# Kernel optimization log

Hardware: AMD Instinct MI355X
Metric: run time of the kernel (lower is better)

## Reference

```python
import jax, jax.numpy as jnp
import numpy as np

ROUTE_SCALE = 2.5
TOP_K = 2
N_EXPERTS = 16


def setup_inputs() -> dict:
    key = jax.random.key(0)
    ks = jax.random.split(key, 8)
    B, T, D, I, E = 2, 1024, 768, 384, N_EXPERTS
    s = 0.02
    return {
        "x": jax.random.normal(ks[0], (B, T, D), dtype=jnp.float32),
        "gate_w": jax.random.normal(ks[1], (E, D), dtype=jnp.float32) * s,
        "sg_w": jax.random.normal(ks[2], (I, D), dtype=jnp.float32) * s,
        "su_w": jax.random.normal(ks[3], (I, D), dtype=jnp.float32) * s,
        "sd_w": jax.random.normal(ks[4], (D, I), dtype=jnp.float32) * s,
        "rg_w": jax.random.normal(ks[5], (E, I, D), dtype=jnp.float32) * s,
        "ru_w": jax.random.normal(ks[6], (E, I, D), dtype=jnp.float32) * s,
        "rd_w": jax.random.normal(ks[7], (E, D, I), dtype=jnp.float32) * s,
    }


def _moe_forward(x, gate_w, sg_w, su_w, sd_w, rg_w, ru_w, rd_w):
    B, T, D = x.shape
    flat = x.reshape(-1, D)  # (N, D), N = B*T

    # ---- shared expert (SwiGLU FFN) ----
    g = flat @ sg_w.T
    u = flat @ su_w.T
    shared_out = (jax.nn.silu(g) * u) @ sd_w.T  # (N, D)

    # ---- gate: softmax(fp32) -> top-k -> renormalize ----
    logits = (flat @ gate_w.T) * ROUTE_SCALE  # (N, E)
    scores = jax.nn.softmax(logits.astype(jnp.float32), axis=-1)
    topk_w, topk_i = jax.lax.top_k(scores, TOP_K)  # (N, K)
    topk_w = topk_w / jnp.sum(topk_w, axis=-1, keepdims=True)
    topk_w = topk_w.astype(x.dtype)

    # aux load-balancing loss
    one_hot = jax.nn.one_hot(topk_i, N_EXPERTS, dtype=jnp.float32)  # (N, K, E)
    mask = one_hot.sum(axis=1)  # (N, E)
    f = mask.mean(axis=0)
    p = scores.mean(axis=0)
    aux_loss = jnp.sum(f * p) * N_EXPERTS

    # combine weights per (token, expert): sum_k w_k * [idx_k == e]
    combine = jnp.einsum("nk,nke->ne", topk_w, one_hot.astype(x.dtype))  # (N, E)

    # ---- routed experts as batched (grouped) SwiGLU GEMMs ----
    rg = jnp.einsum("nd,eid->nei", flat, rg_w)  # (N, E, I)
    ru = jnp.einsum("nd,eid->nei", flat, ru_w)
    rh = jax.nn.silu(rg) * ru  # (N, E, I)
    eo = jnp.einsum("nei,edi->ned", rh, rd_w)  # (N, E, D)
    routed_out = jnp.einsum("ned,ne->nd", eo, combine)  # (N, D)

    out = (shared_out + routed_out).reshape(B, T, D)
    return out, aux_loss


def reference(x, gate_w, sg_w, su_w, sd_w, rg_w, ru_w, rd_w):
    return _moe_forward(x, gate_w, sg_w, su_w, sd_w, rg_w, ru_w, rd_w)
```

## Files before the change

### kernel.cpp

```cpp
#include <hip/hip_runtime.h>
#include <math.h>

#define NTOK 2048
#define DDIM 768
#define IDIM 384
#define NEXP 16
#define ECAP 2048
#define HSHARED (NEXP * ECAP)
#define GBLK (NTOK / 4)

#define MT 64
#define NSHT2 32
#define NRT2 80
#define NW2 ((NSHT2 + NRT2) * 6)
#define CH2 (NW2 / 8)

#define CR_Z0 1
#define CR_X0 (CR_Z0 + 384)
#define CR_W10 (CR_X0 + 192)
#define CR_WD0 (CR_W10 + 816)
#define CR_END (CR_WD0 + 816)

typedef __attribute__((ext_vector_type(8))) short short8;
typedef __attribute__((ext_vector_type(4))) float f32x4;

__device__ __forceinline__ unsigned short f2bf(float f) {
    unsigned int u = __float_as_uint(f);
    unsigned int r = (u + 0x7fffu + ((u >> 16) & 1u)) >> 16;
    return (unsigned short)r;
}

__device__ __forceinline__ void gload16(const void* g, void* l) {
    __builtin_amdgcn_global_load_lds(
        (const __attribute__((address_space(1))) void*)g,
        (__attribute__((address_space(3))) void*)l, 16, 0, 0);
}

#define WS_XB   1048576u
#define WS_W1F  4194304u
#define WS_WDF  24248320u
#define WS_H    34275328u

__global__ __launch_bounds__(256) void gate_kernel(
    const float* __restrict__ x, const float* __restrict__ gate_w,
    int* __restrict__ topk_i, float* __restrict__ topk_w,
    float* __restrict__ p_partial) {
    __shared__ float p_blk[16];
    int tid = threadIdx.x;
    if (tid < 16) p_blk[tid] = 0.f;
    __syncthreads();

    int wave = tid >> 6, lane = tid & 63;
    int n = blockIdx.x * 4 + wave;
    int e = lane >> 2, q = lane & 3;
    const float4* xr = (const float4*)(x + (size_t)n * DDIM);
    const float4* wr = (const float4*)(gate_w + (size_t)e * DDIM);
    float s = 0.f;
    #pragma unroll 4
    for (int k = q * 48; k < q * 48 + 48; ++k) {
        float4 a = xr[k], b = wr[k];
        s += a.x * b.x + a.y * b.y + a.z * b.z + a.w * b.w;
    }
    s += __shfl_xor(s, 1);
    s += __shfl_xor(s, 2);
    float logit = s * 2.5f;

    float m = logit;
    #pragma unroll
    for (int mask = 4; mask < 64; mask <<= 1)
        m = fmaxf(m, __shfl_xor(m, mask));
    float ex = __expf(logit - m);
    float sum = ex;
    #pragma unroll
    for (int mask = 4; mask < 64; mask <<= 1)
        sum += __shfl_xor(sum, mask);
    float sc = ex / sum;

    float v = sc; int idx = e;
    #pragma unroll
    for (int mask = 4; mask < 64; mask <<= 1) {
        float ov = __shfl_xor(v, mask);
        int   oi = __shfl_xor(idx, mask);
        if (ov > v || (ov == v && oi < idx)) { v = ov; idx = oi; }
    }
    float b0 = v; int i0 = idx;
    v = (e == i0) ? -1.f : sc; idx = e;
    #pragma unroll
    for (int mask = 4; mask < 64; mask <<= 1) {
        float ov = __shfl_xor(v, mask);
        int   oi = __shfl_xor(idx, mask);
        if (ov > v || (ov == v && oi < idx)) { v = ov; idx = oi; }
    }
    float b1 = v; int i1 = idx;
    float rs = 1.f / (b0 + b1);

    if (lane == 0) {
        topk_i[n * 2] = i0; topk_i[n * 2 + 1] = i1;
        topk_w[n * 2] = b0 * rs; topk_w[n * 2 + 1] = b1 * rs;
    }
    if (q == 0) atomicAdd(&p_blk[e], sc);
    __syncthreads();
    if (tid < 16) p_partial[blockIdx.x * 16 + tid] = p_blk[tid];
}

__global__ __launch_bounds__(256) void convroute_kernel(
    const float* __restrict__ x,
    const float* __restrict__ rgw, const float* __restrict__ ruw,
    const float* __restrict__ sgw, const float* __restrict__ suw,
    const float* __restrict__ rdw, const float* __restrict__ sdw,
    float4* __restrict__ out4,
    unsigned short* __restrict__ xb, unsigned short* __restrict__ w1f,
    unsigned short* __restrict__ wdf,
    const int* __restrict__ topk_i, const float* __restrict__ topk_w,
    const float* __restrict__ p_partial,
    int* __restrict__ counts, int* __restrict__ perm_t, float* __restrict__ perm_w,
    float* __restrict__ out_aux) {
    __shared__ unsigned short sbuf[16 * 780];
    int b = blockIdx.x, tid = threadIdx.x;

    if (b == 0) {
        float* s_p    = (float*)sbuf;
        float* s_psum = s_p + 256;
        int*   s_cnt  = (int*)(s_psum + 16);
        int*   s_cur  = s_cnt + 16;
        {
            int e = tid & 15, g = tid >> 4;
            float acc = 0.f;
            for (int bb = g; bb < GBLK; bb += 16) acc += p_partial[bb * 16 + e];
            s_p[tid] = acc;
        }
        if (tid < 16) { s_cnt[tid] = 0; s_cur[tid] = 0; }
        __syncthreads();
        if (tid < 16) {
            float a = 0.f;
            #pragma unroll
            for (int g = 0; g < 16; ++g) a += s_p[g * 16 + tid];
            s_psum[tid] = a;
        }
        for (int n = tid; n < NTOK; n += 256) {
            atomicAdd(&s_cnt[topk_i[n * 2]], 1);
            atomicAdd(&s_cnt[topk_i[n * 2 + 1]], 1);
        }
        __syncthreads();
        if (tid < 16) counts[tid] = s_cnt[tid];
        if (tid == 0) {
            float a = 0.f;
            for (int e = 0; e < 16; ++e) a += (float)s_cnt[e] * s_psum[e];
            out_aux[0] = a * 16.f / ((float)NTOK * (float)NTOK);
        }
        for (int n = tid; n < NTOK; n += 256) {
            #pragma unroll
            for (int k = 0; k < 2; ++k) {
                int e = topk_i[n * 2 + k];
                int pos = atomicAdd(&s_cur[e], 1);
                perm_t[e * ECAP + pos] = n;
                perm_w[e * ECAP + pos] = topk_w[n * 2 + k];
            }
        }
        return;
    }

    if (b < CR_X0) {
        float4 z = make_float4(0.f, 0.f, 0.f, 0.f);
        float4* dst = out4 + (b - CR_Z0) * 1024 + tid;
        #pragma unroll
        for (int j = 0; j < 4; ++j) dst[j * 256] = z;
        return;
    }

    if (b < CR_W10) {
        int bb = b - CR_X0;
        #pragma unroll
        for (int j = 0; j < 4; ++j) {
            int i = bb * 1024 + j * 256 + tid;
            const float* s = x + (size_t)i * 8;
            float4 v0 = *(const float4*)s, v1 = *(const float4*)(s + 4);
            short8 o;
            o[0]=f2bf(v0.x); o[1]=f2bf(v0.y); o[2]=f2bf(v0.z); o[3]=f2bf(v0.w);
            o[4]=f2bf(v1.x); o[5]=f2bf(v1.y); o[6]=f2bf(v1.z); o[7]=f2bf(v1.w);
            *(short8*)(xb + (size_t)i * 8) = o;
        }
        return;
    }

    if (b < CR_WD0) {
        int bb = b - CR_W10;
        int E = bb / 48, rg = bb % 48;
        const float* gsrc_ = (E == 16) ? sgw : rgw + (size_t)E * (IDIM * DDIM);
        const float* usrc_ = (E == 16) ? suw : ruw + (size_t)E * (IDIM * DDIM);
        const float* src = ((rg & 1) ? usrc_ : gsrc_) + (size_t)(rg >> 1) * 16 * DDIM;
        #pragma unroll
        for (int i = 0; i < 12; ++i) {
            int idx = i * 256 + tid;
            int r = idx / 192, c4 = idx - r * 192;
            float4 v = ((const float4*)(src + (size_t)r * DDIM))[c4];
            ushort4 o4;
            o4.x = f2bf(v.x); o4.y = f2bf(v.y); o4.z = f2bf(v.z); o4.w = f2bf(v.w);
            *(ushort4*)(sbuf + r * 780 + c4 * 4) = o4;
        }
        __syncthreads();
        unsigned short* wbase = w1f + (size_t)E * (DDIM * DDIM) + (size_t)rg * 24 * 512;
        #pragma unroll
        for (int c = 0; c < 6; ++c) {
            int cc = c * 256 + tid;
            int ks = cc >> 6, l = cc & 63;
            short8 v8 = *(const short8*)(sbuf + (l & 15) * 780 + ks * 32 + (l >> 4) * 8);
            *(short8*)(wbase + (size_t)(ks * 64 + l) * 8) = v8;
        }
        return;
    }

    {
        int bb = b - CR_WD0;
        int E = bb / 48, cg = bb % 48;
        const float* src = ((E == 16) ? sdw : rdw + (size_t)E * (DDIM * IDIM))
                         + (size_t)cg * 16 * IDIM;
        #pragma unroll
        for (int i = 0; i < 6; ++i) {
            int idx = i * 256 + tid;
            int r = idx / 96, c4 = idx - r * 96;
            float4 v = ((const float4*)(src + (size_t)r * IDIM))[c4];
            ushort4 o4;
            o4.x = f2bf(v.x); o4.y = f2bf(v.y); o4.z = f2bf(v.z); o4.w = f2bf(v.w);
            *(ushort4*)(sbuf + r * 390 + c4 * 4) = o4;
        }
        __syncthreads();
        unsigned short* wbase = wdf + (size_t)E * (DDIM * IDIM) + (size_t)cg * 12 * 512;
        #pragma unroll
        for (int c = 0; c < 3; ++c) {
            int cc = c * 256 + tid;
            int ks = cc >> 6, l = cc & 63;
            short8 v8 = *(const short8*)(sbuf + (l & 15) * 390 + ks * 32 + (l >> 4) * 8);
            *(short8*)(wbase + (size_t)(ks * 64 + l) * 8) = v8;
        }
    }
}

__device__ __forceinline__ void swz_decode(int lid, int& bx, int& y) {
    int wid = (lid & 7) * CH2 + (lid >> 3);
    bx = wid / 6;
    y = wid - bx * 6;
}

__device__ __forceinline__ bool tile_decode(const int* __restrict__ counts,
                                            int r, int& e, int& t, int& cnt) {
    int acc = 0;
    for (int ee = 0; ee < NEXP; ++ee) {
        int c = counts[ee];
        int tiles = (c + 63) >> 6;
        if (r < acc + tiles) { e = ee; t = r - acc; cnt = c; return true; }
        acc += tiles;
    }
    return false;
}

__global__ __launch_bounds__(256, 4) void p1_kernel(
    const unsigned short* __restrict__ xb, const unsigned short* __restrict__ w1f,
    const int* __restrict__ counts, const int* __restrict__ perm_t,
    unsigned short* __restrict__ h) {
    __shared__ unsigned short xs[24 * 512];
    __shared__ int s_tok[MT];

    int tid = threadIdx.x;
    int bx, y;
    swz_decode(blockIdx.x, bx, y);
    int e, hbase;
    if (bx < NSHT2) {
        e = 16;
        hbase = HSHARED + bx * MT;
        if (tid < MT) s_tok[tid] = bx * MT + tid;
    } else {
        int t, cnt;
        if (!tile_decode(counts, bx - NSHT2, e, t, cnt)) return;
        hbase = e * ECAP + t * MT;
        if (tid < MT) {
            int slot = t * MT + tid;
            s_tok[tid] = (slot < cnt) ? perm_t[e * ECAP + slot] : 0;
        }
    }
    __syncthreads();

    int lane = tid & 63, wave = tid >> 6;
    int lr = lane & 15, kg8 = (lane >> 4) * 8, jrow = (lane >> 4) * 4;

    const unsigned short* gsrc = xb + (size_t)s_tok[wave * 16 + lr] * DDIM + kg8;

    const unsigned short* pg = w1f + ((((size_t)e * 48 + (y * 8 + wave * 2    )) * 24) * 64 + lane) * 8;
    const unsigned short* pu = w1f + ((((size_t)e * 48 + (y * 8 + wave * 2 + 1)) * 24) * 64 + lane) * 8;

    f32x4 ag0 = (f32x4)0.f, ag1 = (f32x4)0.f, ag2 = (f32x4)0.f, ag3 = (f32x4)0.f;
    f32x4 au0 = (f32x4)0.f, au1 = (f32x4)0.f, au2 = (f32x4)0.f, au3 = (f32x4)0.f;

    for (int ch = 0; ch < 4; ++ch) {
        if (ch) __syncthreads();
        #pragma unroll
        for (int c = 0; c < 6; ++c)
            gload16(gsrc + (ch * 6 + c) * 32, &xs[(wave * 6 + c) * 512]);
        __syncthreads();

        #pragma unroll
        for (int ksl = 0; ksl < 6; ++ksl) {
            int ksg = ch * 6 + ksl;
            short8 bg = *(const short8*)(pg + (size_t)ksg * 512);
            short8 bu = *(const short8*)(pu + (size_t)ksg * 512);
            short8 a0 = *(const short8*)(xs + (     ksl) * 512 + lane * 8);
            short8 a1 = *(const short8*)(xs + ( 6 + ksl) * 512 + lane * 8);
            short8 a2 = *(const short8*)(xs + (12 + ksl) * 512 + lane * 8);
            short8 a3 = *(const short8*)(xs + (18 + ksl) * 512 + lane * 8);
            ag0 = __builtin_amdgcn_mfma_f32_16x16x32_bf16(a0, bg, ag0, 0, 0, 0);
            au0 = __builtin_amdgcn_mfma_f32_16x16x32_bf16(a0, bu, au0, 0, 0, 0);
            ag1 = __builtin_amdgcn_mfma_f32_16x16x32_bf16(a1, bg, ag1, 0, 0, 0);
            au1 = __builtin_amdgcn_mfma_f32_16x16x32_bf16(a1, bu, au1, 0, 0, 0);
            ag2 = __builtin_amdgcn_mfma_f32_16x16x32_bf16(a2, bg, ag2, 0, 0, 0);
            au2 = __builtin_amdgcn_mfma_f32_16x16x32_bf16(a2, bu, au2, 0, 0, 0);
            ag3 = __builtin_amdgcn_mfma_f32_16x16x32_bf16(a3, bg, ag3, 0, 0, 0);
            au3 = __builtin_amdgcn_mfma_f32_16x16x32_bf16(a3, bu, au3, 0, 0, 0);
        }
    }

    int colg = y * 64 + wave * 16 + lr;
    #pragma unroll
    for (int mf = 0; mf < 4; ++mf) {
        f32x4 g4 = (mf == 0) ? ag0 : (mf == 1) ? ag1 : (mf == 2) ? ag2 : ag3;
        f32x4 u4 = (mf == 0) ? au0 : (mf == 1) ? au1 : (mf == 2) ? au2 : au3;
        #pragma unroll
        for (int j = 0; j < 4; ++j) {
            int tl = mf * 16 + jrow + j;
            float g = g4[j], u = u4[j];
            float hv = g / (1.f + __expf(-g)) * u;
            h[(size_t)(hbase + tl) * IDIM + colg] = f2bf(hv);
        }
    }
}

__global__ __launch_bounds__(256, 4) void p2_kernel(
    const unsigned short* __restrict__ h, const unsigned short* __restrict__ wdf,
    const int* __restrict__ counts,
    const int* __restrict__ perm_t, const float* __restrict__ perm_w,
    float* __restrict__ out) {
    __shared__ unsigned short hs[24 * 512];
    __shared__ int   s_tok[MT];
    __shared__ float s_w[MT];

    int tid = threadIdx.x;
    int bx, y;
    swz_decode(blockIdx.x, bx, y);
    int e, hbase;
    if (bx < NSHT2) {
        e = 16;
        hbase = HSHARED + bx * MT;
        if (tid < MT) { s_tok[tid] = bx * MT + tid; s_w[tid] = 1.f; }
    } else {
        int t, cnt;
        if (!tile_decode(counts, bx - NSHT2, e, t, cnt)) return;
        hbase = e * ECAP + t * MT;
        if (tid < MT) {
            int slot = t * MT + tid;
            bool v = slot < cnt;
            s_tok[tid] = v ? perm_t[e * ECAP + slot] : 0;
            s_w[tid]   = v ? perm_w[e * ECAP + slot] : 0.f;
        }
    }
    __syncthreads();

    int lane = tid & 63, wave = tid >> 6;
    int lr = lane & 15, kg8 = (lane >> 4) * 8, jrow = (lane >> 4) * 4;

    const unsigned short* gsrc = h + (size_t)(hbase + wave * 16 + lr) * IDIM + kg8;

    const unsigned short* p0 = wdf + ((((size_t)e * 48 + (y * 8 + wave * 2    )) * 12) * 64 + lane) * 8;
    const unsigned short* p1 = wdf + ((((size_t)e * 48 + (y * 8 + wave * 2 + 1)) * 12) * 64 + lane) * 8;

    f32x4 c00 = (f32x4)0.f, c01 = (f32x4)0.f, c02 = (f32x4)0.f, c03 = (f32x4)0.f;
    f32x4 c10 = (f32x4)0.f, c11 = (f32x4)0.f, c12 = (f32x4)0.f, c13 = (f32x4)0.f;

    for (int ch = 0; ch < 2; ++ch) {
        if (ch) __syncthreads();
        #pragma unroll
        for (int c = 0; c < 6; ++c)
            gload16(gsrc + (ch * 6 + c) * 32, &hs[(wave * 6 + c) * 512]);
        __syncthreads();

        #pragma unroll
        for (int ksl = 0; ksl < 6; ++ksl) {
            int ksg = ch * 6 + ksl;
            short8 b0 = *(const short8*)(p0 + (size_t)ksg * 512);
            short8 b1 = *(const short8*)(p1 + (size_t)ksg * 512);
            short8 a0 = *(const short8*)(hs + (     ksl) * 512 + lane * 8);
            short8 a1 = *(const short8*)(hs + ( 6 + ksl) * 512 + lane * 8);
            short8 a2 = *(const short8*)(hs + (12 + ksl) * 512 + lane * 8);
            short8 a3 = *(const short8*)(hs + (18 + ksl) * 512 + lane * 8);
            c00 = __builtin_amdgcn_mfma_f32_16x16x32_bf16(a0, b0, c00, 0, 0, 0);
            c10 = __builtin_amdgcn_mfma_f32_16x16x32_bf16(a0, b1, c10, 0, 0, 0);
            c01 = __builtin_amdgcn_mfma_f32_16x16x32_bf16(a1, b0, c01, 0, 0, 0);
            c11 = __builtin_amdgcn_mfma_f32_16x16x32_bf16(a1, b1, c11, 0, 0, 0);
            c02 = __builtin_amdgcn_mfma_f32_16x16x32_bf16(a2, b0, c02, 0, 0, 0);
            c12 = __builtin_amdgcn_mfma_f32_16x16x32_bf16(a2, b1, c12, 0, 0, 0);
            c03 = __builtin_amdgcn_mfma_f32_16x16x32_bf16(a3, b0, c03, 0, 0, 0);
            c13 = __builtin_amdgcn_mfma_f32_16x16x32_bf16(a3, b1, c13, 0, 0, 0);
        }
    }

    int col0 = y * 128 + wave * 32 + lr;
    #pragma unroll
    for (int mf = 0; mf < 4; ++mf) {
        f32x4 v0 = (mf == 0) ? c00 : (mf == 1) ? c01 : (mf == 2) ? c02 : c03;
        f32x4 v1 = (mf == 0) ? c10 : (mf == 1) ? c11 : (mf == 2) ? c12 : c13;
        #pragma unroll
        for (int j = 0; j < 4; ++j) {
            int tl = mf * 16 + jrow + j;
            float w = s_w[tl];
            if (w == 0.f) continue;
            float* orow = out + (size_t)s_tok[tl] * DDIM;
            atomicAdd(orow + col0,      w * v0[j]);
            atomicAdd(orow + col0 + 16, w * v1[j]);
        }
    }
}

extern "C" void kernel_launch(void* const* d_in, const int* in_sizes, int n_in,
                              void* d_out, int out_size, void* d_ws, size_t ws_size,
                              hipStream_t stream) {
    const float* x      = (const float*)d_in[0];
    const float* gate_w = (const float*)d_in[1];
    const float* sg_w   = (const float*)d_in[2];
    const float* su_w   = (const float*)d_in[3];
    const float* sd_w   = (const float*)d_in[4];
    const float* rg_w   = (const float*)d_in[5];
    const float* ru_w   = (const float*)d_in[6];
    const float* rd_w   = (const float*)d_in[7];
    float* out = (float*)d_out;

    char* ws = (char*)d_ws;
    int*   counts    = (int*)(ws + 0);
    int*   perm_t    = (int*)(ws + 1024);
    float* perm_w    = (float*)(ws + 132096);
    float* p_partial = (float*)(ws + 263168);
    int*   topk_i    = (int*)(ws + 295936);
    float* topk_w    = (float*)(ws + 312320);
    unsigned short* xb  = (unsigned short*)(ws + WS_XB);
    unsigned short* w1f = (unsigned short*)(ws + WS_W1F);
    unsigned short* wdf = (unsigned short*)(ws + WS_WDF);
    unsigned short* hbuf= (unsigned short*)(ws + WS_H);

    gate_kernel<<<GBLK, 256, 0, stream>>>(x, gate_w, topk_i, topk_w, p_partial);

    convroute_kernel<<<CR_END, 256, 0, stream>>>(
        x, rg_w, ru_w, sg_w, su_w, rd_w, sd_w,
        (float4*)out, xb, w1f, wdf,
        topk_i, topk_w, p_partial, counts, perm_t, perm_w,
        out + (size_t)NTOK * DDIM);

    p1_kernel<<<NW2, 256, 0, stream>>>(xb, w1f, counts, perm_t, hbuf);

    p2_kernel<<<NW2, 256, 0, stream>>>(hbuf, wdf, counts, perm_t, perm_w, out);
}
```

Baseline: 97.37 us.

## Load GEMM A-operands directly from global memory instead of staging through LDS

Both expert GEMM kernels stop copying the token/activation tile into shared memory with global_load_lds and barriers. Each wave now reads its A fragments straight from global memory, with the K loop fully unrolled. This removes the LDS staging, the __syncthreads and the LDS footprint, which may raise occupancy. In exchange every wave redundantly fetches the same 64-row A tile from global/L2, which raises cache traffic fourfold for the A operand.

```diff
diff --git a/kernel.cpp b/kernel.cpp
--- a/kernel.cpp
+++ b/kernel.cpp
@@ -28,12 +28,6 @@
     unsigned int u = __float_as_uint(f);
     unsigned int r = (u + 0x7fffu + ((u >> 16) & 1u)) >> 16;
     return (unsigned short)r;
-}
-
-__device__ __forceinline__ void gload16(const void* g, void* l) {
-    __builtin_amdgcn_global_load_lds(
-        (const __attribute__((address_space(1))) void*)g,
-        (__attribute__((address_space(3))) void*)l, 16, 0, 0);
 }
 
 #define WS_XB   1048576u
@@ -258,7 +252,6 @@
     const unsigned short* __restrict__ xb, const unsigned short* __restrict__ w1f,
     const int* __restrict__ counts, const int* __restrict__ perm_t,
     unsigned short* __restrict__ h) {
-    __shared__ unsigned short xs[24 * 512];
     __shared__ int s_tok[MT];
 
     int tid = threadIdx.x;
@@ -283,7 +276,10 @@
     int lane = tid & 63, wave = tid >> 6;
     int lr = lane & 15, kg8 = (lane >> 4) * 8, jrow = (lane >> 4) * 4;
 
-    const unsigned short* gsrc = xb + (size_t)s_tok[wave * 16 + lr] * DDIM + kg8;
+    const unsigned short* pa0 = xb + (size_t)s_tok[     lr] * DDIM + kg8;
+    const unsigned short* pa1 = xb + (size_t)s_tok[16 + lr] * DDIM + kg8;
+    const unsigned short* pa2 = xb + (size_t)s_tok[32 + lr] * DDIM + kg8;
+    const unsigned short* pa3 = xb + (size_t)s_tok[48 + lr] * DDIM + kg8;
 
     const unsigned short* pg = w1f + ((((size_t)e * 48 + (y * 8 + wave * 2    )) * 24) * 64 + lane) * 8;
     const unsigned short* pu = w1f + ((((size_t)e * 48 + (y * 8 + wave * 2 + 1)) * 24) * 64 + lane) * 8;
@@ -291,31 +287,22 @@
     f32x4 ag0 = (f32x4)0.f, ag1 = (f32x4)0.f, ag2 = (f32x4)0.f, ag3 = (f32x4)0.f;
     f32x4 au0 = (f32x4)0.f, au1 = (f32x4)0.f, au2 = (f32x4)0.f, au3 = (f32x4)0.f;
 
-    for (int ch = 0; ch < 4; ++ch) {
-        if (ch) __syncthreads();
-        #pragma unroll
-        for (int c = 0; c < 6; ++c)
-            gload16(gsrc + (ch * 6 + c) * 32, &xs[(wave * 6 + c) * 512]);
-        __syncthreads();
-
-        #pragma unroll
-        for (int ksl = 0; ksl < 6; ++ksl) {
-            int ksg = ch * 6 + ksl;
-            short8 bg = *(const short8*)(pg + (size_t)ksg * 512);
-            short8 bu = *(const short8*)(pu + (size_t)ksg * 512);
-            short8 a0 = *(const short8*)(xs + (     ksl) * 512 + lane * 8);
-            short8 a1 = *(const short8*)(xs + ( 6 + ksl) * 512 + lane * 8);
-            short8 a2 = *(const short8*)(xs + (12 + ksl) * 512 + lane * 8);
-            short8 a3 = *(const short8*)(xs + (18 + ksl) * 512 + lane * 8);
-            ag0 = __builtin_amdgcn_mfma_f32_16x16x32_bf16(a0, bg, ag0, 0, 0, 0);
-            au0 = __builtin_amdgcn_mfma_f32_16x16x32_bf16(a0, bu, au0, 0, 0, 0);
-            ag1 = __builtin_amdgcn_mfma_f32_16x16x32_bf16(a1, bg, ag1, 0, 0, 0);
-            au1 = __builtin_amdgcn_mfma_f32_16x16x32_bf16(a1, bu, au1, 0, 0, 0);
-            ag2 = __builtin_amdgcn_mfma_f32_16x16x32_bf16(a2, bg, ag2, 0, 0, 0);
-            au2 = __builtin_amdgcn_mfma_f32_16x16x32_bf16(a2, bu, au2, 0, 0, 0);
-            ag3 = __builtin_amdgcn_mfma_f32_16x16x32_bf16(a3, bg, ag3, 0, 0, 0);
-            au3 = __builtin_amdgcn_mfma_f32_16x16x32_bf16(a3, bu, au3, 0, 0, 0);
-        }
+    #pragma unroll
+    for (int ks = 0; ks < 24; ++ks) {
+        short8 bg = *(const short8*)(pg + (size_t)ks * 512);
+        short8 bu = *(const short8*)(pu + (size_t)ks * 512);
+        short8 a0 = *(const short8*)(pa0 + ks * 32);
+        short8 a1 = *(const short8*)(pa1 + ks * 32);
+        short8 a2 = *(const short8*)(pa2 + ks * 32);
+        short8 a3 = *(const short8*)(pa3 + ks * 32);
+        ag0 = __builtin_amdgcn_mfma_f32_16x16x32_bf16(a0, bg, ag0, 0, 0, 0);
+        au0 = __builtin_amdgcn_mfma_f32_16x16x32_bf16(a0, bu, au0, 0, 0, 0);
+        ag1 = __builtin_amdgcn_mfma_f32_16x16x32_bf16(a1, bg, ag1, 0, 0, 0);
+        au1 = __builtin_amdgcn_mfma_f32_16x16x32_bf16(a1, bu, au1, 0, 0, 0);
+        ag2 = __builtin_amdgcn_mfma_f32_16x16x32_bf16(a2, bg, ag2, 0, 0, 0);
+        au2 = __builtin_amdgcn_mfma_f32_16x16x32_bf16(a2, bu, au2, 0, 0, 0);
+        ag3 = __builtin_amdgcn_mfma_f32_16x16x32_bf16(a3, bg, ag3, 0, 0, 0);
+        au3 = __builtin_amdgcn_mfma_f32_16x16x32_bf16(a3, bu, au3, 0, 0, 0);
     }
 
     int colg = y * 64 + wave * 16 + lr;
@@ -338,7 +325,6 @@
     const int* __restrict__ counts,
     const int* __restrict__ perm_t, const float* __restrict__ perm_w,
     float* __restrict__ out) {
-    __shared__ unsigned short hs[24 * 512];
     __shared__ int   s_tok[MT];
     __shared__ float s_w[MT];
 
@@ -366,7 +352,10 @@
     int lane = tid & 63, wave = tid >> 6;
     int lr = lane & 15, kg8 = (lane >> 4) * 8, jrow = (lane >> 4) * 4;
 
-    const unsigned short* gsrc = h + (size_t)(hbase + wave * 16 + lr) * IDIM + kg8;
+    const unsigned short* pa0 = h + (size_t)(hbase +      lr) * IDIM + kg8;
+    const unsigned short* pa1 = h + (size_t)(hbase + 16 + lr) * IDIM + kg8;
+    const unsigned short* pa2 = h + (size_t)(hbase + 32 + lr) * IDIM + kg8;
+    const unsigned short* pa3 = h + (size_t)(hbase + 48 + lr) * IDIM + kg8;
 
     const unsigned short* p0 = wdf + ((((size_t)e * 48 + (y * 8 + wave * 2    )) * 12) * 64 + lane) * 8;
     const unsigned short* p1 = wdf + ((((size_t)e * 48 + (y * 8 + wave * 2 + 1)) * 12) * 64 + lane) * 8;
@@ -374,31 +363,22 @@
     f32x4 c00 = (f32x4)0.f, c01 = (f32x4)0.f, c02 = (f32x4)0.f, c03 = (f32x4)0.f;
     f32x4 c10 = (f32x4)0.f, c11 = (f32x4)0.f, c12 = (f32x4)0.f, c13 = (f32x4)0.f;
 
-    for (int ch = 0; ch < 2; ++ch) {
-        if (ch) __syncthreads();
-        #pragma unroll
-        for (int c = 0; c < 6; ++c)
-            gload16(gsrc + (ch * 6 + c) * 32, &hs[(wave * 6 + c) * 512]);
-        __syncthreads();
-
-        #pragma unroll
-        for (int ksl = 0; ksl < 6; ++ksl) {
-            int ksg = ch * 6 + ksl;
-            short8 b0 = *(const short8*)(p0 + (size_t)ksg * 512);
-            short8 b1 = *(const short8*)(p1 + (size_t)ksg * 512);
-            short8 a0 = *(const short8*)(hs + (     ksl) * 512 + lane * 8);
-            short8 a1 = *(const short8*)(hs + ( 6 + ksl) * 512 + lane * 8);
-            short8 a2 = *(const short8*)(hs + (12 + ksl) * 512 + lane * 8);
-            short8 a3 = *(const short8*)(hs + (18 + ksl) * 512 + lane * 8);
-            c00 = __builtin_amdgcn_mfma_f32_16x16x32_bf16(a0, b0, c00, 0, 0, 0);
-            c10 = __builtin_amdgcn_mfma_f32_16x16x32_bf16(a0, b1, c10, 0, 0, 0);
-            c01 = __builtin_amdgcn_mfma_f32_16x16x32_bf16(a1, b0, c01, 0, 0, 0);
-            c11 = __builtin_amdgcn_mfma_f32_16x16x32_bf16(a1, b1, c11, 0, 0, 0);
-            c02 = __builtin_amdgcn_mfma_f32_16x16x32_bf16(a2, b0, c02, 0, 0, 0);
-            c12 = __builtin_amdgcn_mfma_f32_16x16x32_bf16(a2, b1, c12, 0, 0, 0);
-            c03 = __builtin_amdgcn_mfma_f32_16x16x32_bf16(a3, b0, c03, 0, 0, 0);
-            c13 = __builtin_amdgcn_mfma_f32_16x16x32_bf16(a3, b1, c13, 0, 0, 0);
-        }
+    #pragma unroll
+    for (int ks = 0; ks < 12; ++ks) {
+        short8 b0 = *(const short8*)(p0 + (size_t)ks * 512);
+        short8 b1 = *(const short8*)(p1 + (size_t)ks * 512);
+        short8 a0 = *(const short8*)(pa0 + ks * 32);
+        short8 a1 = *(const short8*)(pa1 + ks * 32);
+        short8 a2 = *(const short8*)(pa2 + ks * 32);
+        short8 a3 = *(const short8*)(pa3 + ks * 32);
+        c00 = __builtin_amdgcn_mfma_f32_16x16x32_bf16(a0, b0, c00, 0, 0, 0);
+        c10 = __builtin_amdgcn_mfma_f32_16x16x32_bf16(a0, b1, c10, 0, 0, 0);
+        c01 = __builtin_amdgcn_mfma_f32_16x16x32_bf16(a1, b0, c01, 0, 0, 0);
+        c11 = __builtin_amdgcn_mfma_f32_16x16x32_bf16(a1, b1, c11, 0, 0, 0);
+        c02 = __builtin_amdgcn_mfma_f32_16x16x32_bf16(a2, b0, c02, 0, 0, 0);
+        c12 = __builtin_amdgcn_mfma_f32_16x16x32_bf16(a2, b1, c12, 0, 0, 0);
+        c03 = __builtin_amdgcn_mfma_f32_16x16x32_bf16(a3, b0, c03, 0, 0, 0);
+        c13 = __builtin_amdgcn_mfma_f32_16x16x32_bf16(a3, b1, c13, 0, 0, 0);
     }
 
     int col0 = y * 128 + wave * 32 + lr;
```

Measured after the change: 122.0 us. +25.4%, slower.

## Halve token tile to 32 rows and restructure GEMM staging in expert kernels

Applied to the files above, without the earlier changes.

Cuts the token tile per block from 64 to 32 and doubles the grid, so there are more, smaller blocks and less padding waste on partially filled expert tiles. The LDS staging is reorganized so pairs of waves load different k-halves of the same 16-token slab, and the K loop now has 2 chunks in p1 and a single chunk in p2. Launch bounds are raised to 6 blocks per CU to raise occupancy. In exchange, each weight fragment loaded from global memory is reused across only 2 token subtiles instead of 4, which increases weight traffic.

```diff
diff --git a/kernel.cpp b/kernel.cpp
--- a/kernel.cpp
+++ b/kernel.cpp
@@ -9,11 +9,12 @@
 #define HSHARED (NEXP * ECAP)
 #define GBLK (NTOK / 4)
 
-#define MT 64
-#define NSHT2 32
-#define NRT2 80
-#define NW2 ((NSHT2 + NRT2) * 6)
-#define CH2 (NW2 / 8)
+#define MT 32
+#define NSHT3 64
+#define NRT3 144
+#define NT3 (NSHT3 + NRT3)
+#define NW3 (NT3 * 6)
+#define CH3 (NW3 / 8)
 
 #define CR_Z0 1
 #define CR_X0 (CR_Z0 + 384)
@@ -237,7 +238,7 @@
 }
 
 __device__ __forceinline__ void swz_decode(int lid, int& bx, int& y) {
-    int wid = (lid & 7) * CH2 + (lid >> 3);
+    int wid = (lid & 7) * CH3 + (lid >> 3);
     bx = wid / 6;
     y = wid - bx * 6;
 }
@@ -247,14 +248,14 @@
     int acc = 0;
     for (int ee = 0; ee < NEXP; ++ee) {
         int c = counts[ee];
-        int tiles = (c + 63) >> 6;
+        int tiles = (c + 31) >> 5;
         if (r < acc + tiles) { e = ee; t = r - acc; cnt = c; return true; }
         acc += tiles;
     }
     return false;
 }
 
-__global__ __launch_bounds__(256, 4) void p1_kernel(
+__global__ __launch_bounds__(256, 6) void p1_kernel(
     const unsigned short* __restrict__ xb, const unsigned short* __restrict__ w1f,
     const int* __restrict__ counts, const int* __restrict__ perm_t,
     unsigned short* __restrict__ h) {
@@ -265,13 +266,13 @@
     int bx, y;
     swz_decode(blockIdx.x, bx, y);
     int e, hbase;
-    if (bx < NSHT2) {
+    if (bx < NSHT3) {
         e = 16;
         hbase = HSHARED + bx * MT;
         if (tid < MT) s_tok[tid] = bx * MT + tid;
     } else {
         int t, cnt;
-        if (!tile_decode(counts, bx - NSHT2, e, t, cnt)) return;
+        if (!tile_decode(counts, bx - NSHT3, e, t, cnt)) return;
         hbase = e * ECAP + t * MT;
         if (tid < MT) {
             int slot = t * MT + tid;
@@ -283,46 +284,44 @@
     int lane = tid & 63, wave = tid >> 6;
     int lr = lane & 15, kg8 = (lane >> 4) * 8, jrow = (lane >> 4) * 4;
 
-    const unsigned short* gsrc = xb + (size_t)s_tok[wave * 16 + lr] * DDIM + kg8;
+    const unsigned short* gsrc = xb
+        + (size_t)s_tok[(wave >> 1) * 16 + lr] * DDIM + kg8;
+    int kslbase = (wave & 1) * 6;
 
     const unsigned short* pg = w1f + ((((size_t)e * 48 + (y * 8 + wave * 2    )) * 24) * 64 + lane) * 8;
     const unsigned short* pu = w1f + ((((size_t)e * 48 + (y * 8 + wave * 2 + 1)) * 24) * 64 + lane) * 8;
 
-    f32x4 ag0 = (f32x4)0.f, ag1 = (f32x4)0.f, ag2 = (f32x4)0.f, ag3 = (f32x4)0.f;
-    f32x4 au0 = (f32x4)0.f, au1 = (f32x4)0.f, au2 = (f32x4)0.f, au3 = (f32x4)0.f;
-
-    for (int ch = 0; ch < 4; ++ch) {
+    f32x4 ag0 = (f32x4)0.f, ag1 = (f32x4)0.f;
+    f32x4 au0 = (f32x4)0.f, au1 = (f32x4)0.f;
+
+    #pragma unroll
+    for (int ch = 0; ch < 2; ++ch) {
         if (ch) __syncthreads();
         #pragma unroll
         for (int c = 0; c < 6; ++c)
-            gload16(gsrc + (ch * 6 + c) * 32, &xs[(wave * 6 + c) * 512]);
+            gload16(gsrc + (ch * 12 + kslbase + c) * 32,
+                    &xs[(wave * 6 + c) * 512]);
         __syncthreads();
 
         #pragma unroll
-        for (int ksl = 0; ksl < 6; ++ksl) {
-            int ksg = ch * 6 + ksl;
+        for (int ksl = 0; ksl < 12; ++ksl) {
+            int ksg = ch * 12 + ksl;
             short8 bg = *(const short8*)(pg + (size_t)ksg * 512);
             short8 bu = *(const short8*)(pu + (size_t)ksg * 512);
             short8 a0 = *(const short8*)(xs + (     ksl) * 512 + lane * 8);
-            short8 a1 = *(const short8*)(xs + ( 6 + ksl) * 512 + lane * 8);
-            short8 a2 = *(const short8*)(xs + (12 + ksl) * 512 + lane * 8);
-            short8 a3 = *(const short8*)(xs + (18 + ksl) * 512 + lane * 8);
+            short8 a1 = *(const short8*)(xs + (12 + ksl) * 512 + lane * 8);
             ag0 = __builtin_amdgcn_mfma_f32_16x16x32_bf16(a0, bg, ag0, 0, 0, 0);
             au0 = __builtin_amdgcn_mfma_f32_16x16x32_bf16(a0, bu, au0, 0, 0, 0);
             ag1 = __builtin_amdgcn_mfma_f32_16x16x32_bf16(a1, bg, ag1, 0, 0, 0);
             au1 = __builtin_amdgcn_mfma_f32_16x16x32_bf16(a1, bu, au1, 0, 0, 0);
-            ag2 = __builtin_amdgcn_mfma_f32_16x16x32_bf16(a2, bg, ag2, 0, 0, 0);
-            au2 = __builtin_amdgcn_mfma_f32_16x16x32_bf16(a2, bu, au2, 0, 0, 0);
-            ag3 = __builtin_amdgcn_mfma_f32_16x16x32_bf16(a3, bg, ag3, 0, 0, 0);
-            au3 = __builtin_amdgcn_mfma_f32_16x16x32_bf16(a3, bu, au3, 0, 0, 0);
         }
     }
 
     int colg = y * 64 + wave * 16 + lr;
     #pragma unroll
-    for (int mf = 0; mf < 4; ++mf) {
-        f32x4 g4 = (mf == 0) ? ag0 : (mf == 1) ? ag1 : (mf == 2) ? ag2 : ag3;
-        f32x4 u4 = (mf == 0) ? au0 : (mf == 1) ? au1 : (mf == 2) ? au2 : au3;
+    for (int mf = 0; mf < 2; ++mf) {
+        f32x4 g4 = mf ? ag1 : ag0;
+        f32x4 u4 = mf ? au1 : au0;
         #pragma unroll
         for (int j = 0; j < 4; ++j) {
             int tl = mf * 16 + jrow + j;
@@ -333,7 +332,7 @@
     }
 }
 
-__global__ __launch_bounds__(256, 4) void p2_kernel(
+__global__ __launch_bounds__(256, 6) void p2_kernel(
     const unsigned short* __restrict__ h, const unsigned short* __restrict__ wdf,
     const int* __restrict__ counts,
     const int* __restrict__ perm_t, const float* __restrict__ perm_w,
@@ -346,13 +345,13 @@
     int bx, y;
     swz_decode(blockIdx.x, bx, y);
     int e, hbase;
-    if (bx < NSHT2) {
+    if (bx < NSHT3) {
         e = 16;
         hbase = HSHARED + bx * MT;
         if (tid < MT) { s_tok[tid] = bx * MT + tid; s_w[tid] = 1.f; }
     } else {
         int t, cnt;
-        if (!tile_decode(counts, bx - NSHT2, e, t, cnt)) return;
+        if (!tile_decode(counts, bx - NSHT3, e, t, cnt)) return;
         hbase = e * ECAP + t * MT;
         if (tid < MT) {
             int slot = t * MT + tid;
@@ -366,46 +365,37 @@
     int lane = tid & 63, wave = tid >> 6;
     int lr = lane & 15, kg8 = (lane >> 4) * 8, jrow = (lane >> 4) * 4;
 
-    const unsigned short* gsrc = h + (size_t)(hbase + wave * 16 + lr) * IDIM + kg8;
+    const unsigned short* gsrc = h
+        + (size_t)(hbase + (wave >> 1) * 16 + lr) * IDIM + kg8;
+    int kslbase = (wave & 1) * 6;
+    #pragma unroll
+    for (int c = 0; c < 6; ++c)
+        gload16(gsrc + (kslbase + c) * 32, &hs[(wave * 6 + c) * 512]);
+    __syncthreads();
 
     const unsigned short* p0 = wdf + ((((size_t)e * 48 + (y * 8 + wave * 2    )) * 12) * 64 + lane) * 8;
     const unsigned short* p1 = wdf + ((((size_t)e * 48 + (y * 8 + wave * 2 + 1)) * 12) * 64 + lane) * 8;
 
-    f32x4 c00 = (f32x4)0.f, c01 = (f32x4)0.f, c02 = (f32x4)0.f, c03 = (f32x4)0.f;
-    f32x4 c10 = (f32x4)0.f, c11 = (f32x4)0.f, c12 = (f32x4)0.f, c13 = (f32x4)0.f;
-
-    for (int ch = 0; ch < 2; ++ch) {
-        if (ch) __syncthreads();
-        #pragma unroll
-        for (int c = 0; c < 6; ++c)
-            gload16(gsrc + (ch * 6 + c) * 32, &hs[(wave * 6 + c) * 512]);
-        __syncthreads();
-
-        #pragma unroll
-        for (int ksl = 0; ksl < 6; ++ksl) {
-            int ksg = ch * 6 + ksl;
-            short8 b0 = *(const short8*)(p0 + (size_t)ksg * 512);
-            short8 b1 = *(const short8*)(p1 + (size_t)ksg * 512);
-            short8 a0 = *(const short8*)(hs + (     ksl) * 512 + lane * 8);
-            short8 a1 = *(const short8*)(hs + ( 6 + ksl) * 512 + lane * 8);
-            short8 a2 = *(const short8*)(hs + (12 + ksl) * 512 + lane * 8);
-            short8 a3 = *(const short8*)(hs + (18 + ksl) * 512 + lane * 8);
-            c00 = __builtin_amdgcn_mfma_f32_16x16x32_bf16(a0, b0, c00, 0, 0, 0);
-            c10 = __builtin_amdgcn_mfma_f32_16x16x32_bf16(a0, b1, c10, 0, 0, 0);
-            c01 = __builtin_amdgcn_mfma_f32_16x16x32_bf16(a1, b0, c01, 0, 0, 0);
-            c11 = __builtin_amdgcn_mfma_f32_16x16x32_bf16(a1, b1, c11, 0, 0, 0);
-            c02 = __builtin_amdgcn_mfma_f32_16x16x32_bf16(a2, b0, c02, 0, 0, 0);
-            c12 = __builtin_amdgcn_mfma_f32_16x16x32_bf16(a2, b1, c12, 0, 0, 0);
-            c03 = __builtin_amdgcn_mfma_f32_16x16x32_bf16(a3, b0, c03, 0, 0, 0);
-            c13 = __builtin_amdgcn_mfma_f32_16x16x32_bf16(a3, b1, c13, 0, 0, 0);
-        }
+    f32x4 c00 = (f32x4)0.f, c01 = (f32x4)0.f;
+    f32x4 c10 = (f32x4)0.f, c11 = (f32x4)0.f;
+
+    #pragma unroll
+    for (int ksl = 0; ksl < 12; ++ksl) {
+        short8 b0 = *(const short8*)(p0 + (size_t)ksl * 512);
+        short8 b1 = *(const short8*)(p1 + (size_t)ksl * 512);
+        short8 a0 = *(const short8*)(hs + (     ksl) * 512 + lane * 8);
+        short8 a1 = *(const short8*)(hs + (12 + ksl) * 512 + lane * 8);
+        c00 = __builtin_amdgcn_mfma_f32_16x16x32_bf16(a0, b0, c00, 0, 0, 0);
+        c10 = __builtin_amdgcn_mfma_f32_16x16x32_bf16(a0, b1, c10, 0, 0, 0);
+        c01 = __builtin_amdgcn_mfma_f32_16x16x32_bf16(a1, b0, c01, 0, 0, 0);
+        c11 = __builtin_amdgcn_mfma_f32_16x16x32_bf16(a1, b1, c11, 0, 0, 0);
     }
 
     int col0 = y * 128 + wave * 32 + lr;
     #pragma unroll
-    for (int mf = 0; mf < 4; ++mf) {
-        f32x4 v0 = (mf == 0) ? c00 : (mf == 1) ? c01 : (mf == 2) ? c02 : c03;
-        f32x4 v1 = (mf == 0) ? c10 : (mf == 1) ? c11 : (mf == 2) ? c12 : c13;
+    for (int mf = 0; mf < 2; ++mf) {
+        f32x4 v0 = mf ? c01 : c00;
+        f32x4 v1 = mf ? c11 : c10;
         #pragma unroll
         for (int j = 0; j < 4; ++j) {
             int tl = mf * 16 + jrow + j;
@@ -451,7 +441,7 @@
         topk_i, topk_w, p_partial, counts, perm_t, perm_w,
         out + (size_t)NTOK * DDIM);
 
-    p1_kernel<<<NW2, 256, 0, stream>>>(xb, w1f, counts, perm_t, hbuf);
-
-    p2_kernel<<<NW2, 256, 0, stream>>>(hbuf, wdf, counts, perm_t, perm_w, out);
-}
+    p1_kernel<<<NW3, 256, 0, stream>>>(xb, w1f, counts, perm_t, hbuf);
+
+    p2_kernel<<<NW3, 256, 0, stream>>>(hbuf, wdf, counts, perm_t, perm_w, out);
+}
```

Result: faster. 95.33 us (-2.1%).
